# Optimization experiments

Hardware: AMD Instinct MI355X
Metric: run time of the kernel (lower is better)

Reference implementation:

```python
import jax, jax.numpy as jnp
import numpy as np

B, S, E, H = 4, 2048, 2048, 16
D = E // H  # head_dim = 128


def setup_inputs() -> dict:
    key = jax.random.key(0)
    ks = jax.random.split(key, 10)
    sc = 1.0 / np.sqrt(E)
    x = jax.random.normal(ks[0], (B, S, E), dtype=jnp.float32)
    causal_mask = jnp.tril(jnp.ones((S, S), dtype=jnp.int32))  # 1 = keep, 0 = mask
    wq = jax.random.normal(ks[1], (E, E), dtype=jnp.float32) * sc
    bq = jax.random.normal(ks[2], (E,), dtype=jnp.float32) * sc
    wk = jax.random.normal(ks[3], (E, E), dtype=jnp.float32) * sc
    bk = jax.random.normal(ks[4], (E,), dtype=jnp.float32) * sc
    wv = jax.random.normal(ks[5], (E, E), dtype=jnp.float32) * sc
    bv = jax.random.normal(ks[6], (E,), dtype=jnp.float32) * sc
    wo = jax.random.normal(ks[7], (E, E), dtype=jnp.float32) * sc
    bo = jax.random.normal(ks[8], (E,), dtype=jnp.float32) * sc
    return {"x": x, "causal_mask": causal_mask, "wq": wq, "bq": bq,
            "wk": wk, "bk": bk, "wv": wv, "bv": bv, "wo": wo, "bo": bo}


def _split_heads(t):
    # [B,S,E] -> [B,H,S,D]
    return t.reshape(B, S, H, D).transpose(0, 2, 1, 3)


def reference(x, causal_mask, wq, bq, wk, bk, wv, bv, wo, bo):
    # torch Linear: y = x @ W.T + b
    q = _split_heads(x @ wq.T + bq)
    k = _split_heads(x @ wk.T + bk)
    v = _split_heads(x @ wv.T + bv)
    scale = 1.0 / jnp.sqrt(jnp.asarray(D, dtype=x.dtype))
    dots = jnp.einsum("bhqd,bhkd->bhqk", q, k) * scale
    dots = jnp.where(causal_mask == 0, jnp.asarray(-jnp.inf, dots.dtype), dots)
    attn = jax.nn.softmax(dots, axis=-1)
    ctx = jnp.einsum("bhqk,bhkd->bhqd", attn, v)
    ctx = ctx.transpose(0, 2, 1, 3).reshape(B, S, E)  # merge heads
    return ctx @ wo.T + bo
```

## Files before the change

kernel.cpp:

```cpp
#include <hip/hip_runtime.h>
#include <hip/hip_bf16.h>

#define B_ 4
#define S_ 2048
#define E_ 2048
#define H_ 16
#define D_ 128
#define M_ (B_*S_)

typedef __attribute__((ext_vector_type(8))) short short8;
typedef __attribute__((ext_vector_type(4))) float f32x4;

__device__ __forceinline__ unsigned short f2bf(float f) {
  union { __hip_bfloat16 h; unsigned short u; } c;
  c.h = __float2bfloat16(f);
  return c.u;
}

__device__ __forceinline__ void gld_lds16(const void* g, void* l) {
  __builtin_amdgcn_global_load_lds((const __attribute__((address_space(1))) void*)g,
                                   (__attribute__((address_space(3))) void*)l, 16, 0, 0);
}

__device__ __forceinline__ float fexp2(float x) {
#if __has_builtin(__builtin_amdgcn_exp2f)
  return __builtin_amdgcn_exp2f(x);
#else
  return exp2f(x);
#endif
}

__global__ __launch_bounds__(256) void cast_bf16_kernel(const float* __restrict__ in,
                                                        unsigned short* __restrict__ out,
                                                        int n4) {
  int i = blockIdx.x * 256 + threadIdx.x;
  if (i >= n4) return;
  float4 v = ((const float4*)in)[i];
  ushort4 o;
  o.x = f2bf(v.x); o.y = f2bf(v.y); o.z = f2bf(v.z); o.w = f2bf(v.w);
  ((ushort4*)out)[i] = o;
}

__global__ __launch_bounds__(256) void cast_w4_kernel(const float* __restrict__ w0,
                                                      const float* __restrict__ w1,
                                                      const float* __restrict__ w2,
                                                      const float* __restrict__ w3,
                                                      unsigned short* __restrict__ o0,
                                                      unsigned short* __restrict__ o1,
                                                      unsigned short* __restrict__ o2,
                                                      unsigned short* __restrict__ o3,
                                                      int n4) {
  int i = blockIdx.x * 256 + threadIdx.x;
  if (i >= n4) return;
  const float* in = (blockIdx.y == 0) ? w0 : (blockIdx.y == 1) ? w1 : (blockIdx.y == 2) ? w2 : w3;
  unsigned short* out = (blockIdx.y == 0) ? o0 : (blockIdx.y == 1) ? o1 : (blockIdx.y == 2) ? o2 : o3;
  float4 v = ((const float4*)in)[i];
  ushort4 o;
  o.x = f2bf(v.x); o.y = f2bf(v.y); o.z = f2bf(v.z); o.w = f2bf(v.w);
  ((ushort4*)out)[i] = o;
}

template <typename OutT, bool TR>
__device__ __forceinline__ void gemm_core(const unsigned short* __restrict__ A,
                                          const unsigned short* __restrict__ W,
                                          const float* __restrict__ bias,
                                          OutT* __restrict__ C,
                                          int M, int N, int K, float oscale,
                                          int m0, int n0,
                                          unsigned short* As, unsigned short* Bs) {
  const int tid  = threadIdx.x;
  const int lane = tid & 63;
  const int wid  = tid >> 6;
  const int wr = (wid >> 2) * 128;
  const int wc = (wid & 3) * 64;
  const int lr  = lane & 15;
  const int lg  = lane >> 4;

  f32x4 acc[8][4];
#pragma unroll
  for (int i = 0; i < 8; i++)
#pragma unroll
    for (int j = 0; j < 4; j++) acc[i][j] = (f32x4){0.f, 0.f, 0.f, 0.f};

  const int rS = tid >> 3;
  const int uS = (tid & 7) ^ (rS & 7);
  const unsigned short* asrc = A + (size_t)(m0 + rS) * K + uS * 8;
  const unsigned short* bsrc = W + (size_t)(n0 + rS) * K + uS * 8;
  char* adst = (char*)As + wid * 1024;
  char* bdst = (char*)Bs + wid * 1024;

  const int swR = (lr & 7) << 4;
  const int nK = K >> 6;

#pragma unroll
  for (int i = 0; i < 4; ++i) {
    gld_lds16(asrc + (size_t)(64 * i) * K, adst + i * 8192);
    gld_lds16(bsrc + (size_t)(64 * i) * K, bdst + i * 8192);
  }

  for (int t = 0; t < nK; ++t) {
    const int bo = (t & 1) * 32768;
    __syncthreads();

    if (t + 1 < nK) {
      const int kt2 = (t + 1) * 64;
      const int nbo = bo ^ 32768;
#pragma unroll
      for (int i = 0; i < 4; ++i) {
        gld_lds16(asrc + kt2 + (size_t)(64 * i) * K, adst + nbo + i * 8192);
        gld_lds16(bsrc + kt2 + (size_t)(64 * i) * K, bdst + nbo + i * 8192);
      }
    }

    const char* AsB = (const char*)As + bo;
    const char* BsB = (const char*)Bs + bo;
#pragma unroll
    for (int kk = 0; kk < 2; kk++) {
      const int cb = ((kk * 4 + lg) << 4) ^ swR;
      short8 bf[4];
#pragma unroll
      for (int j = 0; j < 4; j++)
        bf[j] = *(const short8*)(BsB + (wc + j * 16 + lr) * 128 + cb);
#pragma unroll
      for (int mh = 0; mh < 2; mh++) {
        short8 af[4];
#pragma unroll
        for (int i = 0; i < 4; i++)
          af[i] = *(const short8*)(AsB + (wr + mh * 64 + i * 16 + lr) * 128 + cb);
        __builtin_amdgcn_s_setprio(1);
#pragma unroll
        for (int i = 0; i < 4; i++)
#pragma unroll
          for (int j = 0; j < 4; j++) {
            if constexpr (TR)
              acc[mh * 4 + i][j] = __builtin_amdgcn_mfma_f32_16x16x32_bf16(bf[j], af[i], acc[mh * 4 + i][j], 0, 0, 0);
            else
              acc[mh * 4 + i][j] = __builtin_amdgcn_mfma_f32_16x16x32_bf16(af[i], bf[j], acc[mh * 4 + i][j], 0, 0, 0);
          }
        __builtin_amdgcn_s_setprio(0);
      }
    }
  }

  if constexpr (TR) {
    const int lg4 = lg * 4;
#pragma unroll
    for (int j = 0; j < 4; j++) {
      const int gn = n0 + wc + j * 16 + lg4;
      const float4 bv4 = *(const float4*)&bias[gn];
#pragma unroll
      for (int i = 0; i < 8; i++) {
        const int gm = m0 + wr + i * 16 + lr;
#pragma unroll
        for (int r = 0; r < 4; r++) {
          const float v = (acc[i][j][r] + ((const float*)&bv4)[r]) * oscale;
          ((unsigned short*)C)[(size_t)(gn + r) * M + gm] = f2bf(v);
        }
      }
    }
  } else {
#pragma unroll
    for (int i = 0; i < 8; i++) {
      const int gm = m0 + wr + i * 16 + lg * 4;
#pragma unroll
      for (int j = 0; j < 4; j++) {
        const int gn = n0 + wc + j * 16 + lr;
        const float bv = bias[gn];
#pragma unroll
        for (int r = 0; r < 4; r++) {
          const float v = (acc[i][j][r] + bv) * oscale;
          if constexpr (sizeof(OutT) == 2)
            ((unsigned short*)C)[(size_t)(gm + r) * N + gn] = f2bf(v);
          else
            ((float*)C)[(size_t)(gm + r) * N + gn] = v;
        }
      }
    }
  }
}

template <typename OutT, bool TR = false>
__global__ __launch_bounds__(512) void gemm_bt256(const unsigned short* __restrict__ A,
                                                  const unsigned short* __restrict__ W,
                                                  const float* __restrict__ bias,
                                                  OutT* __restrict__ C,
                                                  int M, int N, int K, float oscale) {
  __shared__ unsigned short As[2 * 256 * 64];
  __shared__ unsigned short Bs[2 * 256 * 64];
  const int nwg = gridDim.x * gridDim.y;
  const int lin = blockIdx.x + gridDim.x * blockIdx.y;
  const int nl  = (lin & 7) * (nwg >> 3) + (lin >> 3);
  const int m0 = (nl / gridDim.x) * 256;
  const int n0 = (nl % gridDim.x) * 256;
  gemm_core<OutT, TR>(A, W, bias, C, M, N, K, oscale, m0, n0, As, Bs);
}

__global__ __launch_bounds__(512) void gemm_qkv(const unsigned short* __restrict__ A,
                                                const unsigned short* __restrict__ Wq,
                                                const unsigned short* __restrict__ Wk,
                                                const unsigned short* __restrict__ Wv,
                                                const float* __restrict__ bq,
                                                const float* __restrict__ bk,
                                                const float* __restrict__ bv,
                                                unsigned short* __restrict__ Qo,
                                                unsigned short* __restrict__ Ko,
                                                unsigned short* __restrict__ VTo,
                                                int M, int N, int K, float qs) {
  __shared__ unsigned short As[2 * 256 * 64];
  __shared__ unsigned short Bs[2 * 256 * 64];
  const int nwg = gridDim.x * gridDim.y;
  const int lin = blockIdx.x + gridDim.x * blockIdx.y;
  const int nl  = (lin & 7) * (nwg >> 3) + (lin >> 3);
  const int ntx = nl % 24;
  const int m0  = (nl / 24) * 256;
  const int wsel = ntx >> 3;
  const int n0  = (ntx & 7) * 256;
  if (wsel == 0)
    gemm_core<unsigned short, false>(A, Wq, bq, Qo, M, N, K, qs,   m0, n0, As, Bs);
  else if (wsel == 1)
    gemm_core<unsigned short, false>(A, Wk, bk, Ko, M, N, K, 1.0f, m0, n0, As, Bs);
  else
    gemm_core<unsigned short, true >(A, Wv, bv, VTo, M, N, K, 1.0f, m0, n0, As, Bs);
}

__global__ __launch_bounds__(256, 4) void flash_attn(const unsigned short* __restrict__ Q,
                                                     const unsigned short* __restrict__ K,
                                                     const unsigned short* __restrict__ VT,
                                                     unsigned short* __restrict__ Ctx) {
  __shared__ unsigned short Ks[64 * 128];
  __shared__ unsigned short Vt[128 * 64];
  __shared__ unsigned short Pl[4 * 1024];

  const int tid  = threadIdx.x;
  const int lane = tid & 63;
  const int wid  = tid >> 6;
  const int lr  = lane & 15;
  const int lg  = lane >> 4;
  const int lk8 = lg * 8;
  const int lin = blockIdx.x + 16 * blockIdx.y + 256 * blockIdx.z;
  const int nl  = (lin & 7) * 128 + (lin >> 3);
  const int bxw = nl & 15;
  const int h   = (nl >> 4) & 15;
  const int b   = nl >> 8;
  const size_t base = ((size_t)b * S_) * E_ + (size_t)h * D_;
  const unsigned short* __restrict__ Kh = K + base;
  const unsigned short* __restrict__ VTh = VT + (size_t)(h * D_) * M_ + (size_t)b * S_;
  unsigned short* Plf = Pl + wid * 1024;

  const int rK = tid >> 4;
  const int cK = ((tid * 16) & 255) ^ ((rK & 7) << 4);
  const unsigned short* ksrcB = Kh + (size_t)rK * E_ + (cK >> 1);
  char* kdstB = (char*)Ks + wid * 1024;

  const int dVb = tid >> 3;
  const int cV  = tid & 7;
  const unsigned short* vsrcB = VTh + (size_t)dVb * M_ + (size_t)((cV ^ (dVb & 7)) * 8);
  char* vdstB = (char*)Vt + wid * 1024;

  const int plw0 = (lg >> 1) * 128 + lr * 8 + (lg & 1) * 4;
  const int plrd = lg * 128 + lr * 8;

#pragma unroll 1
  for (int half = 0; half < 2; ++half) {
    const int ti = half ? (31 - bxw) : bxw;
    const int qblk = ti * 64;
    const int q0w  = qblk + wid * 16;
    const int qrow = q0w + lr;

    short8 qf[4];
#pragma unroll
    for (int kk = 0; kk < 4; kk++)
      qf[kk] = *(const short8*)&Q[base + (size_t)qrow * E_ + kk * 32 + lk8];

    f32x4 o[8];
#pragma unroll
    for (int d0 = 0; d0 < 8; d0++) o[d0] = (f32x4){0.f, 0.f, 0.f, 0.f};
    float mrow = -INFINITY;
    float lsum = 0.f;

    const int nt = ti + 1;

    for (int t = 0; t < nt; ++t) {
      const int kv0 = t * 64;
      const size_t koff = (size_t)kv0 * E_;

#pragma unroll
      for (int p = 0; p < 4; ++p) {
        gld_lds16(ksrcB + koff + (size_t)(16 * p) * E_, kdstB + p * 4096);
        gld_lds16(vsrcB + (size_t)(32 * p) * M_ + kv0,  vdstB + p * 4096);
      }
      __syncthreads();

      f32x4 s[4];
#pragma unroll
      for (int c = 0; c < 4; c++) s[c] = (f32x4){0.f, 0.f, 0.f, 0.f};
      const int swK = (lr & 7) << 4;
      __builtin_amdgcn_s_setprio(1);
#pragma unroll
      for (int kk = 0; kk < 4; kk++) {
        const int cb = (kk * 64 + lg * 16) ^ swK;
#pragma unroll
        for (int c = 0; c < 4; c++) {
          const short8 kf = *(const short8*)((const char*)Ks + (c * 16 + lr) * 256 + cb);
          s[c] = __builtin_amdgcn_mfma_f32_16x16x32_bf16(kf, qf[kk], s[c], 0, 0, 0);
        }
      }
      __builtin_amdgcn_s_setprio(0);

      float v[4][4];
#pragma unroll
      for (int c = 0; c < 4; c++)
#pragma unroll
        for (int r = 0; r < 4; r++) v[c][r] = s[c][r];
      if (t == nt - 1) {
#pragma unroll
        for (int c = 0; c < 4; c++) {
          const int kvq = kv0 + c * 16 + lg * 4;
#pragma unroll
          for (int r = 0; r < 4; r++)
            if (kvq + r > qrow) v[c][r] = -INFINITY;
        }
      }

      float pm = fmaxf(fmaxf(fmaxf(v[0][0], v[0][1]), fmaxf(v[0][2], v[0][3])),
                       fmaxf(fmaxf(v[1][0], v[1][1]), fmaxf(v[1][2], v[1][3])));
      pm = fmaxf(pm, fmaxf(fmaxf(fmaxf(v[2][0], v[2][1]), fmaxf(v[2][2], v[2][3])),
                           fmaxf(fmaxf(v[3][0], v[3][1]), fmaxf(v[3][2], v[3][3]))));
      pm = fmaxf(pm, __shfl_xor(pm, 16));
      pm = fmaxf(pm, __shfl_xor(pm, 32));

      const float need = pm - mrow;
      if (!__all(need <= 8.f)) {
        const float mnew = fmaxf(mrow, pm);
        const float al = fexp2(mrow - mnew);
        lsum *= al;
#pragma unroll
        for (int d0 = 0; d0 < 8; ++d0) {
          f32x4 tt = o[d0];
          tt[0] *= al; tt[1] *= al; tt[2] *= al; tt[3] *= al;
          o[d0] = tt;
        }
        mrow = mnew;
      }

      ushort4 wpk[4];
      float ps = 0.f;
#pragma unroll
      for (int c = 0; c < 4; c++) {
        const float e0 = fexp2(v[c][0] - mrow);
        const float e1 = fexp2(v[c][1] - mrow);
        const float e2 = fexp2(v[c][2] - mrow);
        const float e3 = fexp2(v[c][3] - mrow);
        wpk[c].x = f2bf(e0); wpk[c].y = f2bf(e1);
        wpk[c].z = f2bf(e2); wpk[c].w = f2bf(e3);
        ps += (e0 + e1) + (e2 + e3);
      }
      lsum += ps;

#pragma unroll
      for (int c = 0; c < 4; c++)
        *(ushort4*)&Plf[plw0 + c * 256] = wpk[c];
      asm volatile("s_waitcnt lgkmcnt(0)" ::: "memory");
      __builtin_amdgcn_sched_barrier(0);

      const short8 pb0 = *(const short8*)&Plf[plrd];
      const short8 pb1 = *(const short8*)&Plf[plrd + 512];
      const int d7 = lr & 7;
      __builtin_amdgcn_s_setprio(1);
#pragma unroll
      for (int d0 = 0; d0 < 8; ++d0) {
        const int d = d0 * 16 + lr;
        const short8 vb0 = *(const short8*)&Vt[d * 64 + ((lg ^ d7) << 3)];
        o[d0] = __builtin_amdgcn_mfma_f32_16x16x32_bf16(vb0, pb0, o[d0], 0, 0, 0);
        const short8 vb1 = *(const short8*)&Vt[d * 64 + (((4 + lg) ^ d7) << 3)];
        o[d0] = __builtin_amdgcn_mfma_f32_16x16x32_bf16(vb1, pb1, o[d0], 0, 0, 0);
      }
      __builtin_amdgcn_s_setprio(0);
      __syncthreads();
    }

    float ls = lsum;
    ls += __shfl_xor(ls, 16);
    ls += __shfl_xor(ls, 32);
    const float inv = 1.0f / ls;
    unsigned short* crow = Ctx + base + (size_t)qrow * E_ + lg * 4;
#pragma unroll
    for (int d0 = 0; d0 < 8; ++d0) {
      ushort4 st;
      st.x = f2bf(o[d0][0] * inv);
      st.y = f2bf(o[d0][1] * inv);
      st.z = f2bf(o[d0][2] * inv);
      st.w = f2bf(o[d0][3] * inv);
      *(ushort4*)&crow[d0 * 16] = st;
    }
  }
}

extern "C" void kernel_launch(void* const* d_in, const int* in_sizes, int n_in,
                              void* d_out, int out_size, void* d_ws, size_t ws_size,
                              hipStream_t stream) {
  const float* x  = (const float*)d_in[0];
  const float* wq = (const float*)d_in[2];
  const float* bq = (const float*)d_in[3];
  const float* wk = (const float*)d_in[4];
  const float* bk = (const float*)d_in[5];
  const float* wv = (const float*)d_in[6];
  const float* bv = (const float*)d_in[7];
  const float* wo = (const float*)d_in[8];
  const float* bo = (const float*)d_in[9];
  float* out = (float*)d_out;

  char* ws = (char*)d_ws;
  const size_t MB = 1024 * 1024;
  unsigned short* xb  = (unsigned short*)(ws);
  unsigned short* wqb = (unsigned short*)(ws + 32 * MB);
  unsigned short* wkb = (unsigned short*)(ws + 40 * MB);
  unsigned short* wvb = (unsigned short*)(ws + 48 * MB);
  unsigned short* wob = (unsigned short*)(ws + 56 * MB);
  unsigned short* Qb  = (unsigned short*)(ws + 64 * MB);
  unsigned short* Kb  = (unsigned short*)(ws + 96 * MB);
  unsigned short* VTb = (unsigned short*)(ws + 128 * MB);
  unsigned short* Cb  = (unsigned short*)(ws + 160 * MB);

  const int nx4 = M_ * E_ / 4;
  const int nw4 = E_ * E_ / 4;
  cast_bf16_kernel<<<nx4 / 256, 256, 0, stream>>>(x, xb, nx4);
  cast_w4_kernel<<<dim3(nw4 / 256, 4), 256, 0, stream>>>(wq, wk, wv, wo,
                                                         wqb, wkb, wvb, wob, nw4);

  const float scale = 0.08838834764831845f * 1.44269504088896340736f;

  gemm_qkv<<<dim3(24, 32), 512, 0, stream>>>(xb, wqb, wkb, wvb, bq, bk, bv,
                                             Qb, Kb, VTb, M_, E_, E_, scale);

  flash_attn<<<dim3(S_ / 64 / 2, H_, B_), 256, 0, stream>>>(Qb, Kb, VTb, Cb);

  gemm_bt256<float><<<dim3(E_ / 256, M_ / 256), 512, 0, stream>>>(Cb, wob, bo, out, M_, E_, E_, 1.0f);
}
```

Baseline: 410.2 us.

## Process two 64-row query groups per flash-attention block to reuse K/V tiles

Each flash-attention workgroup now handles a 128-row query block: every wave keeps two 16-row query fragments with separate softmax state and accumulators, and each K/V tile loaded into LDS feeds both. This halves K/V global-to-LDS traffic and barrier count per unit of work and launches half as many blocks. On the last tile only the second group is computed, since the first group is entirely masked there. The cost is roughly double the register use (launch bounds lowered from 4 to 2 waves per SIMD, so occupancy may fall), larger LDS for P, and fewer blocks, which may worsen load balance across CUs.

```diff
diff --git a/kernel.cpp b/kernel.cpp
--- a/kernel.cpp
+++ b/kernel.cpp
@@ -223,13 +223,13 @@
     gemm_core<unsigned short, true >(A, Wv, bv, VTo, M, N, K, 1.0f, m0, n0, As, Bs);
 }
 
-__global__ __launch_bounds__(256, 4) void flash_attn(const unsigned short* __restrict__ Q,
+__global__ __launch_bounds__(256, 2) void flash_attn(const unsigned short* __restrict__ Q,
                                                      const unsigned short* __restrict__ K,
                                                      const unsigned short* __restrict__ VT,
                                                      unsigned short* __restrict__ Ctx) {
   __shared__ unsigned short Ks[64 * 128];
   __shared__ unsigned short Vt[128 * 64];
-  __shared__ unsigned short Pl[4 * 1024];
+  __shared__ unsigned short Pl[4 * 2048];
 
   const int tid  = threadIdx.x;
   const int lane = tid & 63;
@@ -237,15 +237,15 @@
   const int lr  = lane & 15;
   const int lg  = lane >> 4;
   const int lk8 = lg * 8;
-  const int lin = blockIdx.x + 16 * blockIdx.y + 256 * blockIdx.z;
-  const int nl  = (lin & 7) * 128 + (lin >> 3);
-  const int bxw = nl & 15;
-  const int h   = (nl >> 4) & 15;
-  const int b   = nl >> 8;
+  const int lin = blockIdx.x + 8 * blockIdx.y + 128 * blockIdx.z;
+  const int nl  = (lin & 7) * 64 + (lin >> 3);
+  const int bxw = nl & 7;
+  const int h   = (nl >> 3) & 15;
+  const int b   = nl >> 7;
   const size_t base = ((size_t)b * S_) * E_ + (size_t)h * D_;
   const unsigned short* __restrict__ Kh = K + base;
   const unsigned short* __restrict__ VTh = VT + (size_t)(h * D_) * M_ + (size_t)b * S_;
-  unsigned short* Plf = Pl + wid * 1024;
+  unsigned short* Plf = Pl + wid * 2048;
 
   const int rK = tid >> 4;
   const int cK = ((tid * 16) & 255) ^ ((rK & 7) << 4);
@@ -262,23 +262,28 @@
 
 #pragma unroll 1
   for (int half = 0; half < 2; ++half) {
-    const int ti = half ? (31 - bxw) : bxw;
-    const int qblk = ti * 64;
-    const int q0w  = qblk + wid * 16;
-    const int qrow = q0w + lr;
-
-    short8 qf[4];
-#pragma unroll
-    for (int kk = 0; kk < 4; kk++)
-      qf[kk] = *(const short8*)&Q[base + (size_t)qrow * E_ + kk * 32 + lk8];
-
-    f32x4 o[8];
-#pragma unroll
-    for (int d0 = 0; d0 < 8; d0++) o[d0] = (f32x4){0.f, 0.f, 0.f, 0.f};
-    float mrow = -INFINITY;
-    float lsum = 0.f;
-
-    const int nt = ti + 1;
+    const int ti = half ? (15 - bxw) : bxw;
+    const int qblk = ti * 128;
+    const int qrow0 = qblk + wid * 16 + lr;
+    const int qrow1 = qrow0 + 64;
+
+    short8 qf0[4], qf1[4];
+#pragma unroll
+    for (int kk = 0; kk < 4; kk++) {
+      qf0[kk] = *(const short8*)&Q[base + (size_t)qrow0 * E_ + kk * 32 + lk8];
+      qf1[kk] = *(const short8*)&Q[base + (size_t)qrow1 * E_ + kk * 32 + lk8];
+    }
+
+    f32x4 o0[8], o1[8];
+#pragma unroll
+    for (int d0 = 0; d0 < 8; d0++) {
+      o0[d0] = (f32x4){0.f, 0.f, 0.f, 0.f};
+      o1[d0] = (f32x4){0.f, 0.f, 0.f, 0.f};
+    }
+    float m0r = -INFINITY, m1r = -INFINITY;
+    float l0 = 0.f, l1 = 0.f;
+
+    const int nt = 2 * ti + 2;
 
     for (int t = 0; t < nt; ++t) {
       const int kv0 = t * 64;
@@ -291,107 +296,204 @@
       }
       __syncthreads();
 
-      f32x4 s[4];
-#pragma unroll
-      for (int c = 0; c < 4; c++) s[c] = (f32x4){0.f, 0.f, 0.f, 0.f};
+      const bool g0act = (t < nt - 1);
+      const bool mk0   = (t == nt - 2);
+      const bool mk1   = (t == nt - 1);
+
+      f32x4 s0[4], s1[4];
+#pragma unroll
+      for (int c = 0; c < 4; c++) {
+        s0[c] = (f32x4){0.f, 0.f, 0.f, 0.f};
+        s1[c] = (f32x4){0.f, 0.f, 0.f, 0.f};
+      }
       const int swK = (lr & 7) << 4;
-      __builtin_amdgcn_s_setprio(1);
-#pragma unroll
-      for (int kk = 0; kk < 4; kk++) {
-        const int cb = (kk * 64 + lg * 16) ^ swK;
+      if (g0act) {
+        __builtin_amdgcn_s_setprio(1);
+#pragma unroll
+        for (int kk = 0; kk < 4; kk++) {
+          const int cb = (kk * 64 + lg * 16) ^ swK;
+#pragma unroll
+          for (int c = 0; c < 4; c++) {
+            const short8 kf = *(const short8*)((const char*)Ks + (c * 16 + lr) * 256 + cb);
+            s1[c] = __builtin_amdgcn_mfma_f32_16x16x32_bf16(kf, qf1[kk], s1[c], 0, 0, 0);
+            s0[c] = __builtin_amdgcn_mfma_f32_16x16x32_bf16(kf, qf0[kk], s0[c], 0, 0, 0);
+          }
+        }
+        __builtin_amdgcn_s_setprio(0);
+      } else {
+        __builtin_amdgcn_s_setprio(1);
+#pragma unroll
+        for (int kk = 0; kk < 4; kk++) {
+          const int cb = (kk * 64 + lg * 16) ^ swK;
+#pragma unroll
+          for (int c = 0; c < 4; c++) {
+            const short8 kf = *(const short8*)((const char*)Ks + (c * 16 + lr) * 256 + cb);
+            s1[c] = __builtin_amdgcn_mfma_f32_16x16x32_bf16(kf, qf1[kk], s1[c], 0, 0, 0);
+          }
+        }
+        __builtin_amdgcn_s_setprio(0);
+      }
+
+      {
+        float v[4][4];
+#pragma unroll
+        for (int c = 0; c < 4; c++)
+#pragma unroll
+          for (int r = 0; r < 4; r++) v[c][r] = s1[c][r];
+        if (mk1) {
+#pragma unroll
+          for (int c = 0; c < 4; c++) {
+            const int kvq = kv0 + c * 16 + lg * 4;
+#pragma unroll
+            for (int r = 0; r < 4; r++)
+              if (kvq + r > qrow1) v[c][r] = -INFINITY;
+          }
+        }
+        float pm = fmaxf(fmaxf(fmaxf(v[0][0], v[0][1]), fmaxf(v[0][2], v[0][3])),
+                         fmaxf(fmaxf(v[1][0], v[1][1]), fmaxf(v[1][2], v[1][3])));
+        pm = fmaxf(pm, fmaxf(fmaxf(fmaxf(v[2][0], v[2][1]), fmaxf(v[2][2], v[2][3])),
+                             fmaxf(fmaxf(v[3][0], v[3][1]), fmaxf(v[3][2], v[3][3]))));
+        pm = fmaxf(pm, __shfl_xor(pm, 16));
+        pm = fmaxf(pm, __shfl_xor(pm, 32));
+        const float need = pm - m1r;
+        if (!__all(need <= 8.f)) {
+          const float mnew = fmaxf(m1r, pm);
+          const float al = fexp2(m1r - mnew);
+          l1 *= al;
+#pragma unroll
+          for (int d0 = 0; d0 < 8; ++d0) {
+            f32x4 tt = o1[d0];
+            tt[0] *= al; tt[1] *= al; tt[2] *= al; tt[3] *= al;
+            o1[d0] = tt;
+          }
+          m1r = mnew;
+        }
+        ushort4 wpk[4];
+        float ps = 0.f;
 #pragma unroll
         for (int c = 0; c < 4; c++) {
-          const short8 kf = *(const short8*)((const char*)Ks + (c * 16 + lr) * 256 + cb);
-          s[c] = __builtin_amdgcn_mfma_f32_16x16x32_bf16(kf, qf[kk], s[c], 0, 0, 0);
-        }
-      }
-      __builtin_amdgcn_s_setprio(0);
-
-      float v[4][4];
-#pragma unroll
-      for (int c = 0; c < 4; c++)
-#pragma unroll
-        for (int r = 0; r < 4; r++) v[c][r] = s[c][r];
-      if (t == nt - 1) {
+          const float e0 = fexp2(v[c][0] - m1r);
+          const float e1 = fexp2(v[c][1] - m1r);
+          const float e2 = fexp2(v[c][2] - m1r);
+          const float e3 = fexp2(v[c][3] - m1r);
+          wpk[c].x = f2bf(e0); wpk[c].y = f2bf(e1);
+          wpk[c].z = f2bf(e2); wpk[c].w = f2bf(e3);
+          ps += (e0 + e1) + (e2 + e3);
+        }
+        l1 += ps;
+#pragma unroll
+        for (int c = 0; c < 4; c++)
+          *(ushort4*)&Plf[1024 + plw0 + c * 256] = wpk[c];
+      }
+
+      if (g0act) {
+        float v[4][4];
+#pragma unroll
+        for (int c = 0; c < 4; c++)
+#pragma unroll
+          for (int r = 0; r < 4; r++) v[c][r] = s0[c][r];
+        if (mk0) {
+#pragma unroll
+          for (int c = 0; c < 4; c++) {
+            const int kvq = kv0 + c * 16 + lg * 4;
+#pragma unroll
+            for (int r = 0; r < 4; r++)
+              if (kvq + r > qrow0) v[c][r] = -INFINITY;
+          }
+        }
+        float pm = fmaxf(fmaxf(fmaxf(v[0][0], v[0][1]), fmaxf(v[0][2], v[0][3])),
+                         fmaxf(fmaxf(v[1][0], v[1][1]), fmaxf(v[1][2], v[1][3])));
+        pm = fmaxf(pm, fmaxf(fmaxf(fmaxf(v[2][0], v[2][1]), fmaxf(v[2][2], v[2][3])),
+                             fmaxf(fmaxf(v[3][0], v[3][1]), fmaxf(v[3][2], v[3][3]))));
+        pm = fmaxf(pm, __shfl_xor(pm, 16));
+        pm = fmaxf(pm, __shfl_xor(pm, 32));
+        const float need = pm - m0r;
+        if (!__all(need <= 8.f)) {
+          const float mnew = fmaxf(m0r, pm);
+          const float al = fexp2(m0r - mnew);
+          l0 *= al;
+#pragma unroll
+          for (int d0 = 0; d0 < 8; ++d0) {
+            f32x4 tt = o0[d0];
+            tt[0] *= al; tt[1] *= al; tt[2] *= al; tt[3] *= al;
+            o0[d0] = tt;
+          }
+          m0r = mnew;
+        }
+        ushort4 wpk[4];
+        float ps = 0.f;
 #pragma unroll
         for (int c = 0; c < 4; c++) {
-          const int kvq = kv0 + c * 16 + lg * 4;
-#pragma unroll
-          for (int r = 0; r < 4; r++)
-            if (kvq + r > qrow) v[c][r] = -INFINITY;
-        }
-      }
-
-      float pm = fmaxf(fmaxf(fmaxf(v[0][0], v[0][1]), fmaxf(v[0][2], v[0][3])),
-                       fmaxf(fmaxf(v[1][0], v[1][1]), fmaxf(v[1][2], v[1][3])));
-      pm = fmaxf(pm, fmaxf(fmaxf(fmaxf(v[2][0], v[2][1]), fmaxf(v[2][2], v[2][3])),
-                           fmaxf(fmaxf(v[3][0], v[3][1]), fmaxf(v[3][2], v[3][3]))));
-      pm = fmaxf(pm, __shfl_xor(pm, 16));
-      pm = fmaxf(pm, __shfl_xor(pm, 32));
-
-      const float need = pm - mrow;
-      if (!__all(need <= 8.f)) {
-        const float mnew = fmaxf(mrow, pm);
-        const float al = fexp2(mrow - mnew);
-        lsum *= al;
-#pragma unroll
-        for (int d0 = 0; d0 < 8; ++d0) {
-          f32x4 tt = o[d0];
-          tt[0] *= al; tt[1] *= al; tt[2] *= al; tt[3] *= al;
-          o[d0] = tt;
-        }
-        mrow = mnew;
-      }
-
-      ushort4 wpk[4];
-      float ps = 0.f;
-#pragma unroll
-      for (int c = 0; c < 4; c++) {
-        const float e0 = fexp2(v[c][0] - mrow);
-        const float e1 = fexp2(v[c][1] - mrow);
-        const float e2 = fexp2(v[c][2] - mrow);
-        const float e3 = fexp2(v[c][3] - mrow);
-        wpk[c].x = f2bf(e0); wpk[c].y = f2bf(e1);
-        wpk[c].z = f2bf(e2); wpk[c].w = f2bf(e3);
-        ps += (e0 + e1) + (e2 + e3);
-      }
-      lsum += ps;
-
-#pragma unroll
-      for (int c = 0; c < 4; c++)
-        *(ushort4*)&Plf[plw0 + c * 256] = wpk[c];
+          const float e0 = fexp2(v[c][0] - m0r);
+          const float e1 = fexp2(v[c][1] - m0r);
+          const float e2 = fexp2(v[c][2] - m0r);
+          const float e3 = fexp2(v[c][3] - m0r);
+          wpk[c].x = f2bf(e0); wpk[c].y = f2bf(e1);
+          wpk[c].z = f2bf(e2); wpk[c].w = f2bf(e3);
+          ps += (e0 + e1) + (e2 + e3);
+        }
+        l0 += ps;
+#pragma unroll
+        for (int c = 0; c < 4; c++)
+          *(ushort4*)&Plf[plw0 + c * 256] = wpk[c];
+      }
+
       asm volatile("s_waitcnt lgkmcnt(0)" ::: "memory");
       __builtin_amdgcn_sched_barrier(0);
 
-      const short8 pb0 = *(const short8*)&Plf[plrd];
-      const short8 pb1 = *(const short8*)&Plf[plrd + 512];
+      const short8 pb1a = *(const short8*)&Plf[1024 + plrd];
+      const short8 pb1b = *(const short8*)&Plf[1024 + plrd + 512];
       const int d7 = lr & 7;
-      __builtin_amdgcn_s_setprio(1);
-#pragma unroll
-      for (int d0 = 0; d0 < 8; ++d0) {
-        const int d = d0 * 16 + lr;
-        const short8 vb0 = *(const short8*)&Vt[d * 64 + ((lg ^ d7) << 3)];
-        o[d0] = __builtin_amdgcn_mfma_f32_16x16x32_bf16(vb0, pb0, o[d0], 0, 0, 0);
-        const short8 vb1 = *(const short8*)&Vt[d * 64 + (((4 + lg) ^ d7) << 3)];
-        o[d0] = __builtin_amdgcn_mfma_f32_16x16x32_bf16(vb1, pb1, o[d0], 0, 0, 0);
-      }
-      __builtin_amdgcn_s_setprio(0);
+      if (g0act) {
+        const short8 pb0a = *(const short8*)&Plf[plrd];
+        const short8 pb0b = *(const short8*)&Plf[plrd + 512];
+        __builtin_amdgcn_s_setprio(1);
+#pragma unroll
+        for (int d0 = 0; d0 < 8; ++d0) {
+          const int d = d0 * 16 + lr;
+          const short8 vb0 = *(const short8*)&Vt[d * 64 + ((lg ^ d7) << 3)];
+          const short8 vb1 = *(const short8*)&Vt[d * 64 + (((4 + lg) ^ d7) << 3)];
+          o1[d0] = __builtin_amdgcn_mfma_f32_16x16x32_bf16(vb0, pb1a, o1[d0], 0, 0, 0);
+          o1[d0] = __builtin_amdgcn_mfma_f32_16x16x32_bf16(vb1, pb1b, o1[d0], 0, 0, 0);
+          o0[d0] = __builtin_amdgcn_mfma_f32_16x16x32_bf16(vb0, pb0a, o0[d0], 0, 0, 0);
+          o0[d0] = __builtin_amdgcn_mfma_f32_16x16x32_bf16(vb1, pb0b, o0[d0], 0, 0, 0);
+        }
+        __builtin_amdgcn_s_setprio(0);
+      } else {
+        __builtin_amdgcn_s_setprio(1);
+#pragma unroll
+        for (int d0 = 0; d0 < 8; ++d0) {
+          const int d = d0 * 16 + lr;
+          const short8 vb0 = *(const short8*)&Vt[d * 64 + ((lg ^ d7) << 3)];
+          const short8 vb1 = *(const short8*)&Vt[d * 64 + (((4 + lg) ^ d7) << 3)];
+          o1[d0] = __builtin_amdgcn_mfma_f32_16x16x32_bf16(vb0, pb1a, o1[d0], 0, 0, 0);
+          o1[d0] = __builtin_amdgcn_mfma_f32_16x16x32_bf16(vb1, pb1b, o1[d0], 0, 0, 0);
+        }
+        __builtin_amdgcn_s_setprio(0);
+      }
       __syncthreads();
     }
 
-    float ls = lsum;
-    ls += __shfl_xor(ls, 16);
-    ls += __shfl_xor(ls, 32);
-    const float inv = 1.0f / ls;
-    unsigned short* crow = Ctx + base + (size_t)qrow * E_ + lg * 4;
+    float ls0 = l0, ls1 = l1;
+    ls0 += __shfl_xor(ls0, 16); ls0 += __shfl_xor(ls0, 32);
+    ls1 += __shfl_xor(ls1, 16); ls1 += __shfl_xor(ls1, 32);
+    const float inv0 = 1.0f / ls0;
+    const float inv1 = 1.0f / ls1;
+    unsigned short* crow0 = Ctx + base + (size_t)qrow0 * E_ + lg * 4;
+    unsigned short* crow1 = Ctx + base + (size_t)qrow1 * E_ + lg * 4;
 #pragma unroll
     for (int d0 = 0; d0 < 8; ++d0) {
-      ushort4 st;
-      st.x = f2bf(o[d0][0] * inv);
-      st.y = f2bf(o[d0][1] * inv);
-      st.z = f2bf(o[d0][2] * inv);
-      st.w = f2bf(o[d0][3] * inv);
-      *(ushort4*)&crow[d0 * 16] = st;
+      ushort4 st0, st1;
+      st0.x = f2bf(o0[d0][0] * inv0);
+      st0.y = f2bf(o0[d0][1] * inv0);
+      st0.z = f2bf(o0[d0][2] * inv0);
+      st0.w = f2bf(o0[d0][3] * inv0);
+      st1.x = f2bf(o1[d0][0] * inv1);
+      st1.y = f2bf(o1[d0][1] * inv1);
+      st1.z = f2bf(o1[d0][2] * inv1);
+      st1.w = f2bf(o1[d0][3] * inv1);
+      *(ushort4*)&crow0[d0 * 16] = st0;
+      *(ushort4*)&crow1[d0 * 16] = st1;
     }
   }
 }
@@ -433,7 +535,7 @@
   gemm_qkv<<<dim3(24, 32), 512, 0, stream>>>(xb, wqb, wkb, wvb, bq, bk, bv,
                                              Qb, Kb, VTb, M_, E_, E_, scale);
 
-  flash_attn<<<dim3(S_ / 64 / 2, H_, B_), 256, 0, stream>>>(Qb, Kb, VTb, Cb);
+  flash_attn<<<dim3(S_ / 128 / 2, H_, B_), 256, 0, stream>>>(Qb, Kb, VTb, Cb);
 
   gemm_bt256<float><<<dim3(E_ / 256, M_ / 256), 512, 0, stream>>>(Cb, wob, bo, out, M_, E_, E_, 1.0f);
 }
```

New measurement: 400.7 us (median of 2 runs). 2.3% less time.
